# Kernel optimization log

Measured on AMD Instinct MI355X. Metric: run time of the kernel, lower is better.

The kernel has to match this reference:

```python
import jax, jax.numpy as jnp
import numpy as np

D_MODEL = 2048
D_INNER = 4096  # d_model * expand_factor
LN_EPS = 1e-5


def setup_inputs() -> dict:
    key = jax.random.key(0)
    k1, k2, k3, k4 = jax.random.split(key, 4)
    B, S = 2, 4096
    x = jax.random.normal(k1, (B, S, D_MODEL), dtype=jnp.float32)
    gamma = jnp.ones((D_MODEL,), dtype=jnp.float32)
    beta = jnp.zeros((D_MODEL,), dtype=jnp.float32)
    # nn.Linear-like small init to keep activations in-range
    W_in = jax.random.normal(k2, (2 * D_INNER, D_MODEL), dtype=jnp.float32) * 0.02
    W_out = jax.random.normal(k3, (D_MODEL, D_INNER), dtype=jnp.float32) * 0.02
    dt_min, dt_max = 0.001, 0.1
    dt = jax.random.uniform(k4, (D_INNER,), dtype=jnp.float32) * (dt_max - dt_min) + dt_min
    return {"x": x, "gamma": gamma, "beta": beta, "W_in": W_in, "W_out": W_out, "dt": dt}


def reference(x, gamma, beta, W_in, W_out, dt):
    # x: [B, S, D_MODEL]
    identity = x
    # LayerNorm over last dim
    mu = jnp.mean(x, axis=-1, keepdims=True)
    var = jnp.mean(jnp.square(x - mu), axis=-1, keepdims=True)
    xn = (x - mu) * jax.lax.rsqrt(var + LN_EPS) * gamma + beta
    # in_proj: [B, S, 2*D_INNER]
    projected = jnp.einsum("bsd,ed->bse", xn, W_in)
    z, gate = jnp.split(projected, 2, axis=-1)
    # z gated by sigmoid of clamped z (clamp only inside sigmoid)
    z_gated = z * jax.nn.sigmoid(jnp.clip(z, -15.0, 15.0))
    # temporal weighting by softmax(-dt) over d_inner
    dt_weights = jax.nn.softmax(-dt)  # [D_INNER]
    z_temporal = z_gated * dt_weights  # broadcast over [B, S, D_INNER]
    # gate path: silu on clamped gate
    output = z_temporal * jax.nn.silu(jnp.clip(gate, -15.0, 15.0))
    # out_proj back to d_model
    output = jnp.einsum("bse,de->bsd", output, W_out)
    return output + identity
```

## Files before the change

kernel.cpp:

```cpp
#include <hip/hip_runtime.h>
#include <cstdint>
#include <cstddef>

#define T_TOK 8192
#define DM    2048
#define DI    4096
#define TWO_DI 8192

typedef __attribute__((ext_vector_type(8))) short bf16x8;
typedef __attribute__((ext_vector_type(4))) float f32x4;

__device__ __forceinline__ unsigned short f2bf(float f) {
  union { float f; unsigned u; } c; c.f = f;
  unsigned u = c.u;
  unsigned r = (u + 0x7fffu + ((u >> 16) & 1u)) >> 16;
  return (unsigned short)r;
}

__global__ __launch_bounds__(256) void ln_kernel(
    const float* __restrict__ x, const float* __restrict__ gamma,
    const float* __restrict__ beta, unsigned short* __restrict__ xn) {
  const int t = blockIdx.x;
  const int tid = threadIdx.x;
  const float* row = x + (size_t)t * DM;
  float4 v0 = reinterpret_cast<const float4*>(row)[tid];
  float4 v1 = reinterpret_cast<const float4*>(row)[tid + 256];
  float s  = v0.x + v0.y + v0.z + v0.w + v1.x + v1.y + v1.z + v1.w;
  float ss = v0.x*v0.x + v0.y*v0.y + v0.z*v0.z + v0.w*v0.w
           + v1.x*v1.x + v1.y*v1.y + v1.z*v1.z + v1.w*v1.w;
  #pragma unroll
  for (int off = 32; off > 0; off >>= 1) {
    s  += __shfl_down(s, off);
    ss += __shfl_down(ss, off);
  }
  __shared__ float red[8];
  __shared__ float mu_s, inv_s;
  if ((tid & 63) == 0) { red[tid >> 6] = s; red[4 + (tid >> 6)] = ss; }
  __syncthreads();
  if (tid == 0) {
    float S  = red[0] + red[1] + red[2] + red[3];
    float SS = red[4] + red[5] + red[6] + red[7];
    float mu  = S * (1.0f / DM);
    float var = SS * (1.0f / DM) - mu * mu;
    mu_s = mu;
    inv_s = rsqrtf(var + 1e-5f);
  }
  __syncthreads();
  const float mu = mu_s, inv = inv_s;
  float4 g0 = reinterpret_cast<const float4*>(gamma)[tid];
  float4 b0 = reinterpret_cast<const float4*>(beta)[tid];
  float4 g1 = reinterpret_cast<const float4*>(gamma)[tid + 256];
  float4 b1 = reinterpret_cast<const float4*>(beta)[tid + 256];
  ushort4 o0, o1;
  o0.x = f2bf((v0.x - mu) * inv * g0.x + b0.x);
  o0.y = f2bf((v0.y - mu) * inv * g0.y + b0.y);
  o0.z = f2bf((v0.z - mu) * inv * g0.z + b0.z);
  o0.w = f2bf((v0.w - mu) * inv * g0.w + b0.w);
  o1.x = f2bf((v1.x - mu) * inv * g1.x + b1.x);
  o1.y = f2bf((v1.y - mu) * inv * g1.y + b1.y);
  o1.z = f2bf((v1.z - mu) * inv * g1.z + b1.z);
  o1.w = f2bf((v1.w - mu) * inv * g1.w + b1.w);
  reinterpret_cast<ushort4*>(xn + (size_t)t * DM)[tid]       = o0;
  reinterpret_cast<ushort4*>(xn + (size_t)t * DM)[tid + 256] = o1;
}

__global__ __launch_bounds__(256) void cvt_both(
    const float* __restrict__ a, unsigned short* __restrict__ oa, int n4a,
    const float* __restrict__ b, unsigned short* __restrict__ ob, int n4b) {
  int i = blockIdx.x * 256 + threadIdx.x;
  const float* src;
  unsigned short* dst;
  int idx;
  if (i < n4a) { src = a; dst = oa; idx = i; }
  else { idx = i - n4a; if (idx >= n4b) return; src = b; dst = ob; }
  float4 v = reinterpret_cast<const float4*>(src)[idx];
  ushort4 o;
  o.x = f2bf(v.x); o.y = f2bf(v.y); o.z = f2bf(v.z); o.w = f2bf(v.w);
  reinterpret_cast<ushort4*>(dst)[idx] = o;
}

__global__ __launch_bounds__(256) void dt_softmax(
    const float* __restrict__ dt, float* __restrict__ w) {
  const int tid = threadIdx.x;
  float e[16];
  float local = 0.f;
  #pragma unroll
  for (int i = 0; i < 16; ++i) {
    float v = __expf(-dt[i * 256 + tid]);
    e[i] = v;
    local += v;
  }
  #pragma unroll
  for (int off = 32; off > 0; off >>= 1) local += __shfl_down(local, off);
  __shared__ float red[4];
  __shared__ float tot;
  if ((tid & 63) == 0) red[tid >> 6] = local;
  __syncthreads();
  if (tid == 0) tot = red[0] + red[1] + red[2] + red[3];
  __syncthreads();
  const float inv = 1.f / tot;
  #pragma unroll
  for (int i = 0; i < 16; ++i) w[i * 256 + tid] = e[i] * inv;
}

__device__ __forceinline__ float actf(float z, float g, float w) {
  float zc = fminf(fmaxf(z, -15.f), 15.f);
  float sz = 1.f / (1.f + __expf(-zc));
  float gc = fminf(fmaxf(g, -15.f), 15.f);
  float sg = 1.f / (1.f + __expf(-gc));
  return z * sz * w * gc * sg;
}

#define BAR()    __builtin_amdgcn_s_barrier()
#define SCHED0() __builtin_amdgcn_sched_barrier(0)
#define PRIO1()  __builtin_amdgcn_s_setprio(1)
#define PRIO0()  __builtin_amdgcn_s_setprio(0)
#define WAIT_LGKM0() asm volatile("s_waitcnt lgkmcnt(0)" ::: "memory")
#define WAIT_VM6()   asm volatile("s_waitcnt vmcnt(6)" ::: "memory")

#define GLD16(gaddr, laddr) __builtin_amdgcn_global_load_lds(                 \
    (const __attribute__((address_space(1))) void*)(gaddr),                   \
    (__attribute__((address_space(3))) void*)(laddr), 16, 0, 0)

#define STAGE(ldsbase, gb, k0) do {                                           \
    GLD16((gb) + sOff  + (k0), &(ldsbase)[tid * 8]);                          \
    GLD16((gb) + sOff2 + (k0), &(ldsbase)[tid * 8 + 4096]);                   \
  } while (0)

#define TAIL() do { BAR(); WAIT_LGKM0(); SCHED0(); } while (0)

#define G1_NKT 32
#define G1_NIT 16

__global__ __launch_bounds__(512, 2) void gemm1_fused8(
    const unsigned short* __restrict__ A, const unsigned short* __restrict__ W,
    const float* __restrict__ dtw, unsigned short* __restrict__ act) {
  __shared__ unsigned short lA [2][256 * 64];
  __shared__ unsigned short lB1[2][128 * 64];
  __shared__ unsigned short lB2[2][128 * 64];

  const int tid  = threadIdx.x;
  const int lane = tid & 63;
  const int wmI  = (tid >> 6) >> 2;
  const int wnI  = (tid >> 6) & 3;
  const int tM = blockIdx.y * 256;
  const int tN = blockIdx.x * 128;

  const int r0   = lane & 15;
  const int hi4  = lane >> 4;
  const int swz0 = (hi4 ^ (r0 & 7)) << 3;
  const int swz1 = swz0 ^ 32;
  const int aRow0 = (wmI * 64 + r0) * 64;
  const int bRow  = (wnI * 32 + r0) * 64;

  const int srow = tid >> 3;
  const int scol = ((tid & 7) ^ (srow & 7)) << 3;
  const size_t sOff  = (size_t)srow * DM + scol;
  const size_t sOff2 = sOff + (size_t)64 * DM;

  const unsigned short* Ab    = A + (size_t)tM * DM;
  const unsigned short* Ab128 = Ab + (size_t)128 * DM;
  const unsigned short* B1b   = W + (size_t)tN * DM;
  const unsigned short* B2b   = W + (size_t)(tN + DI) * DM;

  f32x4 accZ[8][2], accG[8][2];
  #pragma unroll
  for (int i = 0; i < 8; ++i)
    #pragma unroll
    for (int j = 0; j < 2; ++j) {
      accZ[i][j] = f32x4{0.f, 0.f, 0.f, 0.f};
      accG[i][j] = f32x4{0.f, 0.f, 0.f, 0.f};
    }
  bf16x8 a0[4][2], a1[4][2], bz[2][2], bg[2][2];

#define G1_LDA0(b) do {                                                       \
    _Pragma("unroll") for (int i = 0; i < 4; ++i) {                           \
      a0[i][0] = *reinterpret_cast<const bf16x8*>(&lA[b][aRow0 + i*1024 + swz0]); \
      a0[i][1] = *reinterpret_cast<const bf16x8*>(&lA[b][aRow0 + i*1024 + swz1]); \
    } } while (0)
#define G1_LDA1(b) do {                                                       \
    _Pragma("unroll") for (int i = 0; i < 4; ++i) {                           \
      a1[i][0] = *reinterpret_cast<const bf16x8*>(&lA[b][8192 + aRow0 + i*1024 + swz0]); \
      a1[i][1] = *reinterpret_cast<const bf16x8*>(&lA[b][8192 + aRow0 + i*1024 + swz1]); \
    } } while (0)
#define G1_LDBZ(b) do {                                                       \
    _Pragma("unroll") for (int j = 0; j < 2; ++j) {                           \
      bz[j][0] = *reinterpret_cast<const bf16x8*>(&lB1[b][bRow + j*1024 + swz0]); \
      bz[j][1] = *reinterpret_cast<const bf16x8*>(&lB1[b][bRow + j*1024 + swz1]); \
    } } while (0)
#define G1_LDBG(b) do {                                                       \
    _Pragma("unroll") for (int j = 0; j < 2; ++j) {                           \
      bg[j][0] = *reinterpret_cast<const bf16x8*>(&lB2[b][bRow + j*1024 + swz0]); \
      bg[j][1] = *reinterpret_cast<const bf16x8*>(&lB2[b][bRow + j*1024 + swz1]); \
    } } while (0)
#define G1_Q(accA, ioff, af) do {                                             \
    PRIO1();                                                                  \
    _Pragma("unroll") for (int kh = 0; kh < 2; ++kh)                          \
      _Pragma("unroll") for (int i = 0; i < 4; ++i)                           \
        _Pragma("unroll") for (int j = 0; j < 2; ++j)                         \
          accA[(ioff)+i][j] = __builtin_amdgcn_mfma_f32_16x16x32_bf16(        \
              af[i][kh], G1_BF[j][kh], accA[(ioff)+i][j], 0, 0, 0);           \
    PRIO0(); SCHED0(); BAR();                                                 \
  } while (0)

  STAGE(lA[0],        Ab,    0);
  STAGE(lB1[0],       B1b,   0);
  STAGE(lB2[0],       B2b,   0);
  STAGE(&lA[0][8192], Ab128, 0);
  STAGE(lA[1],        Ab,    64);
  STAGE(lB1[1],       B1b,   64);
  STAGE(lB2[1],       B2b,   64);
  WAIT_VM6();
  BAR();

  #pragma unroll 1
  for (int t = 0; t < G1_NIT; ++t) {
    const int k1  = (2 * t + 1) * 64;
    const int kt2 = 2 * t + 2;
    const int kt3 = 2 * t + 3;
    const int k2 = (kt2 < G1_NKT ? kt2 : G1_NKT - 1) * 64;
    const int k3 = (kt3 < G1_NKT ? kt3 : G1_NKT - 1) * 64;

#define G1_BF bz
    G1_LDA0(0); G1_LDBZ(0);
    STAGE(&lA[1][8192], Ab128, k1);
    TAIL(); G1_Q(accZ, 0, a0);
#undef G1_BF
#define G1_BF bg
    G1_LDBG(0);
    STAGE(lA[0], Ab, k2);
    TAIL(); G1_Q(accG, 0, a0);
    G1_LDA1(0);
    STAGE(lB1[0], B1b, k2);
    TAIL(); G1_Q(accG, 4, a1);
#undef G1_BF
#define G1_BF bz
    STAGE(lB2[0], B2b, k2);
    WAIT_VM6();
    TAIL(); G1_Q(accZ, 4, a1);
#undef G1_BF

#define G1_BF bz
    G1_LDA0(1); G1_LDBZ(1);
    STAGE(&lA[0][8192], Ab128, k2);
    TAIL(); G1_Q(accZ, 0, a0);
#undef G1_BF
#define G1_BF bg
    G1_LDBG(1);
    STAGE(lA[1], Ab, k3);
    TAIL(); G1_Q(accG, 0, a0);
    G1_LDA1(1);
    STAGE(lB1[1], B1b, k3);
    TAIL(); G1_Q(accG, 4, a1);
#undef G1_BF
#define G1_BF bz
    STAGE(lB2[1], B2b, k3);
    WAIT_VM6();
    TAIL(); G1_Q(accZ, 4, a1);
#undef G1_BF
  }

  const int qr   = hi4 << 2;
  const int colb = tN + wnI * 32 + r0;
  const float w0 = dtw[colb];
  const float w1 = dtw[colb + 16];
  #pragma unroll
  for (int i = 0; i < 8; ++i) {
    const int rowb = tM + wmI * 64 + ((i & 3) << 4) + ((i >> 2) << 7) + qr;
    #pragma unroll
    for (int r = 0; r < 4; ++r) {
      const size_t base = (size_t)(rowb + r) * DI + colb;
      act[base]      = f2bf(actf(accZ[i][0][r], accG[i][0][r], w0));
      act[base + 16] = f2bf(actf(accZ[i][1][r], accG[i][1][r], w1));
    }
  }
#undef G1_LDA0
#undef G1_LDA1
#undef G1_LDBZ
#undef G1_LDBG
#undef G1_Q
}

#define G2_NKT 64
#define G2_NIT 32

__global__ __launch_bounds__(512, 2) void gemm2_res8(
    const unsigned short* __restrict__ A, const unsigned short* __restrict__ Bm,
    float* __restrict__ out, const float* __restrict__ ident) {
  __shared__ unsigned short lA[2][256 * 64];
  __shared__ unsigned short lB[2][256 * 64];

  const int tid  = threadIdx.x;
  const int lane = tid & 63;
  const int wmI  = (tid >> 6) >> 2;
  const int wnI  = (tid >> 6) & 3;
  const int tM = blockIdx.y * 256;
  const int tN = blockIdx.x * 256;

  const int r0   = lane & 15;
  const int hi4  = lane >> 4;
  const int swz0 = (hi4 ^ (r0 & 7)) << 3;
  const int swz1 = swz0 ^ 32;
  const int aRow0 = (wmI * 64 + r0) * 64;
  const int bRow  = (wnI * 32 + r0) * 64;

  const int srow = tid >> 3;
  const int scol = ((tid & 7) ^ (srow & 7)) << 3;
  const size_t sOff  = (size_t)srow * DI + scol;
  const size_t sOff2 = sOff + (size_t)64 * DI;

  const unsigned short* Ab    = A + (size_t)tM * DI;
  const unsigned short* Ab128 = Ab + (size_t)128 * DI;
  const unsigned short* Bb    = Bm + (size_t)tN * DI;
  const unsigned short* Bb128 = Bb + (size_t)128 * DI;

  f32x4 acc[8][4];
  #pragma unroll
  for (int i = 0; i < 8; ++i)
    #pragma unroll
    for (int j = 0; j < 4; ++j) acc[i][j] = f32x4{0.f, 0.f, 0.f, 0.f};
  bf16x8 a0[4][2], a1[4][2], b0[2][2], b1[2][2];

#define G2_LDA0(b) do {                                                       \
    _Pragma("unroll") for (int i = 0; i < 4; ++i) {                           \
      a0[i][0] = *reinterpret_cast<const bf16x8*>(&lA[b][aRow0 + i*1024 + swz0]); \
      a0[i][1] = *reinterpret_cast<const bf16x8*>(&lA[b][aRow0 + i*1024 + swz1]); \
    } } while (0)
#define G2_LDA1(b) do {                                                       \
    _Pragma("unroll") for (int i = 0; i < 4; ++i) {                           \
      a1[i][0] = *reinterpret_cast<const bf16x8*>(&lA[b][8192 + aRow0 + i*1024 + swz0]); \
      a1[i][1] = *reinterpret_cast<const bf16x8*>(&lA[b][8192 + aRow0 + i*1024 + swz1]); \
    } } while (0)
#define G2_LDB0(b) do {                                                       \
    _Pragma("unroll") for (int j = 0; j < 2; ++j) {                           \
      b0[j][0] = *reinterpret_cast<const bf16x8*>(&lB[b][bRow + j*1024 + swz0]); \
      b0[j][1] = *reinterpret_cast<const bf16x8*>(&lB[b][bRow + j*1024 + swz1]); \
    } } while (0)
#define G2_LDB1(b) do {                                                       \
    _Pragma("unroll") for (int j = 0; j < 2; ++j) {                           \
      b1[j][0] = *reinterpret_cast<const bf16x8*>(&lB[b][8192 + bRow + j*1024 + swz0]); \
      b1[j][1] = *reinterpret_cast<const bf16x8*>(&lB[b][8192 + bRow + j*1024 + swz1]); \
    } } while (0)
#define G2_Q(ioff, joff, af, bf) do {                                         \
    PRIO1();                                                                  \
    _Pragma("unroll") for (int kh = 0; kh < 2; ++kh)                          \
      _Pragma("unroll") for (int i = 0; i < 4; ++i)                           \
        _Pragma("unroll") for (int j = 0; j < 2; ++j)                         \
          acc[(ioff)+i][(joff)+j] = __builtin_amdgcn_mfma_f32_16x16x32_bf16(  \
              af[i][kh], bf[j][kh], acc[(ioff)+i][(joff)+j], 0, 0, 0);        \
    PRIO0(); SCHED0(); BAR();                                                 \
  } while (0)

  STAGE(lA[0],        Ab,    0);
  STAGE(lB[0],        Bb,    0);
  STAGE(&lB[0][8192], Bb128, 0);
  STAGE(&lA[0][8192], Ab128, 0);
  STAGE(lA[1],        Ab,    64);
  STAGE(lB[1],        Bb,    64);
  STAGE(&lB[1][8192], Bb128, 64);
  WAIT_VM6();
  BAR();

  #pragma unroll 1
  for (int t = 0; t < G2_NIT; ++t) {
    const int k1  = (2 * t + 1) * 64;
    const int kt2 = 2 * t + 2;
    const int kt3 = 2 * t + 3;
    const int k2 = (kt2 < G2_NKT ? kt2 : G2_NKT - 1) * 64;
    const int k3 = (kt3 < G2_NKT ? kt3 : G2_NKT - 1) * 64;

    G2_LDA0(0); G2_LDB0(0);
    STAGE(&lA[1][8192], Ab128, k1);
    TAIL(); G2_Q(0, 0, a0, b0);
    G2_LDB1(0);
    STAGE(lA[0], Ab, k2);
    TAIL(); G2_Q(0, 2, a0, b1);
    G2_LDA1(0);
    STAGE(lB[0], Bb, k2);
    TAIL(); G2_Q(4, 2, a1, b1);
    STAGE(&lB[0][8192], Bb128, k2);
    WAIT_VM6();
    TAIL(); G2_Q(4, 0, a1, b0);

    G2_LDA0(1); G2_LDB0(1);
    STAGE(&lA[0][8192], Ab128, k2);
    TAIL(); G2_Q(0, 0, a0, b0);
    G2_LDB1(1);
    STAGE(lA[1], Ab, k3);
    TAIL(); G2_Q(0, 2, a0, b1);
    G2_LDA1(1);
    STAGE(lB[1], Bb, k3);
    TAIL(); G2_Q(4, 2, a1, b1);
    STAGE(&lB[1][8192], Bb128, k3);
    WAIT_VM6();
    TAIL(); G2_Q(4, 0, a1, b0);
  }

  const int qr   = hi4 << 2;
  const int colb = tN + wnI * 32 + r0;
  #pragma unroll
  for (int i = 0; i < 8; ++i) {
    const int rowb = tM + wmI * 64 + ((i & 3) << 4) + ((i >> 2) << 7) + qr;
    #pragma unroll
    for (int r = 0; r < 4; ++r) {
      const size_t rowoff = (size_t)(rowb + r) * DM;
      #pragma unroll
      for (int j = 0; j < 4; ++j) {
        const size_t idx = rowoff + colb + ((j & 1) << 4) + ((j >> 1) << 7);
        out[idx] = acc[i][j][r] + ident[idx];
      }
    }
  }
#undef G2_LDA0
#undef G2_LDA1
#undef G2_LDB0
#undef G2_LDB1
#undef G2_Q
}

extern "C" void kernel_launch(void* const* d_in, const int* in_sizes, int n_in,
                              void* d_out, int out_size, void* d_ws, size_t ws_size,
                              hipStream_t stream) {
  const float* x     = (const float*)d_in[0];
  const float* gamma = (const float*)d_in[1];
  const float* beta  = (const float*)d_in[2];
  const float* W_in  = (const float*)d_in[3];
  const float* W_out = (const float*)d_in[4];
  const float* dt    = (const float*)d_in[5];
  float* out = (float*)d_out;

  char* ws = (char*)d_ws;
  unsigned short* xn     = (unsigned short*)(ws);
  unsigned short* win_b  = (unsigned short*)(ws + ((size_t)32 << 20));
  unsigned short* wout_b = (unsigned short*)(ws + ((size_t)64 << 20));
  float*          dtw    = (float*)(ws + ((size_t)80 << 20));
  unsigned short* act    = (unsigned short*)(ws + ((size_t)96 << 20));

  const int n4_in  = TWO_DI * DM / 4;
  const int n4_out = DM * DI / 4;

  ln_kernel<<<T_TOK, 256, 0, stream>>>(x, gamma, beta, xn);
  cvt_both<<<(n4_in + n4_out + 255) / 256, 256, 0, stream>>>(
      W_in, win_b, n4_in, W_out, wout_b, n4_out);
  dt_softmax<<<1, 256, 0, stream>>>(dt, dtw);

  gemm1_fused8<<<dim3(DI / 128, T_TOK / 256), 512, 0, stream>>>(
      xn, win_b, dtw, act);

  gemm2_res8<<<dim3(DM / 256, T_TOK / 256), 512, 0, stream>>>(
      act, wout_b, out, x);
}
```

Before: 586.9 us.

## Split LDS fragment loads by k-half with partial lgkmcnt waits in both GEMMs

Both GEMM kernels now issue LDS fragment reads per k-half. Each quarter waits only on the lgkmcnt needed for the first half of its MFMAs, so those MFMAs can start while the second-half reads are still in flight. The barrier that sat before the LDS wait is also dropped, leaving one barrier per quarter after compute instead of two. This is meant to hide LDS read latency and cut barrier stalls. The risk is that the hand-tuned wait counts must match the compiler's issued instruction order, or the reordering may not help.

After: 602.5 us. +2.6%, slower.

```diff
diff --git a/kernel.cpp b/kernel.cpp
--- a/kernel.cpp
+++ b/kernel.cpp
@@ -115,7 +115,7 @@
 #define SCHED0() __builtin_amdgcn_sched_barrier(0)
 #define PRIO1()  __builtin_amdgcn_s_setprio(1)
 #define PRIO0()  __builtin_amdgcn_s_setprio(0)
-#define WAIT_LGKM0() asm volatile("s_waitcnt lgkmcnt(0)" ::: "memory")
+#define WAIT_LGKM(n) asm volatile("s_waitcnt lgkmcnt(" #n ")" ::: "memory")
 #define WAIT_VM6()   asm volatile("s_waitcnt vmcnt(6)" ::: "memory")
 
 #define GLD16(gaddr, laddr) __builtin_amdgcn_global_load_lds(                 \
@@ -126,8 +126,6 @@
     GLD16((gb) + sOff  + (k0), &(ldsbase)[tid * 8]);                          \
     GLD16((gb) + sOff2 + (k0), &(ldsbase)[tid * 8 + 4096]);                   \
   } while (0)
-
-#define TAIL() do { BAR(); WAIT_LGKM0(); SCHED0(); } while (0)
 
 #define G1_NKT 32
 #define G1_NIT 16
@@ -173,34 +171,33 @@
     }
   bf16x8 a0[4][2], a1[4][2], bz[2][2], bg[2][2];
 
-#define G1_LDA0(b) do {                                                       \
-    _Pragma("unroll") for (int i = 0; i < 4; ++i) {                           \
-      a0[i][0] = *reinterpret_cast<const bf16x8*>(&lA[b][aRow0 + i*1024 + swz0]); \
-      a0[i][1] = *reinterpret_cast<const bf16x8*>(&lA[b][aRow0 + i*1024 + swz1]); \
-    } } while (0)
-#define G1_LDA1(b) do {                                                       \
-    _Pragma("unroll") for (int i = 0; i < 4; ++i) {                           \
-      a1[i][0] = *reinterpret_cast<const bf16x8*>(&lA[b][8192 + aRow0 + i*1024 + swz0]); \
-      a1[i][1] = *reinterpret_cast<const bf16x8*>(&lA[b][8192 + aRow0 + i*1024 + swz1]); \
-    } } while (0)
-#define G1_LDBZ(b) do {                                                       \
-    _Pragma("unroll") for (int j = 0; j < 2; ++j) {                           \
-      bz[j][0] = *reinterpret_cast<const bf16x8*>(&lB1[b][bRow + j*1024 + swz0]); \
-      bz[j][1] = *reinterpret_cast<const bf16x8*>(&lB1[b][bRow + j*1024 + swz1]); \
-    } } while (0)
-#define G1_LDBG(b) do {                                                       \
-    _Pragma("unroll") for (int j = 0; j < 2; ++j) {                           \
-      bg[j][0] = *reinterpret_cast<const bf16x8*>(&lB2[b][bRow + j*1024 + swz0]); \
-      bg[j][1] = *reinterpret_cast<const bf16x8*>(&lB2[b][bRow + j*1024 + swz1]); \
-    } } while (0)
-#define G1_Q(accA, ioff, af) do {                                             \
+#define G1_LDA0K(b, kh) do {                                                  \
+    _Pragma("unroll") for (int i = 0; i < 4; ++i)                             \
+      a0[i][kh] = *reinterpret_cast<const bf16x8*>(                           \
+          &lA[b][aRow0 + i*1024 + ((kh) ? swz1 : swz0)]);                     \
+  } while (0)
+#define G1_LDA1K(b, kh) do {                                                  \
+    _Pragma("unroll") for (int i = 0; i < 4; ++i)                             \
+      a1[i][kh] = *reinterpret_cast<const bf16x8*>(                           \
+          &lA[b][8192 + aRow0 + i*1024 + ((kh) ? swz1 : swz0)]);              \
+  } while (0)
+#define G1_LDBZK(b, kh) do {                                                  \
+    _Pragma("unroll") for (int j = 0; j < 2; ++j)                             \
+      bz[j][kh] = *reinterpret_cast<const bf16x8*>(                           \
+          &lB1[b][bRow + j*1024 + ((kh) ? swz1 : swz0)]);                     \
+  } while (0)
+#define G1_LDBGK(b, kh) do {                                                  \
+    _Pragma("unroll") for (int j = 0; j < 2; ++j)                             \
+      bg[j][kh] = *reinterpret_cast<const bf16x8*>(                           \
+          &lB2[b][bRow + j*1024 + ((kh) ? swz1 : swz0)]);                     \
+  } while (0)
+#define G1_H(accA, ioff, af, bf, kh) do {                                     \
     PRIO1();                                                                  \
-    _Pragma("unroll") for (int kh = 0; kh < 2; ++kh)                          \
-      _Pragma("unroll") for (int i = 0; i < 4; ++i)                           \
-        _Pragma("unroll") for (int j = 0; j < 2; ++j)                         \
-          accA[(ioff)+i][j] = __builtin_amdgcn_mfma_f32_16x16x32_bf16(        \
-              af[i][kh], G1_BF[j][kh], accA[(ioff)+i][j], 0, 0, 0);           \
-    PRIO0(); SCHED0(); BAR();                                                 \
+    _Pragma("unroll") for (int i = 0; i < 4; ++i)                             \
+      _Pragma("unroll") for (int j = 0; j < 2; ++j)                           \
+        accA[(ioff)+i][j] = __builtin_amdgcn_mfma_f32_16x16x32_bf16(          \
+            af[i][kh], bf[j][kh], accA[(ioff)+i][j], 0, 0, 0);                \
+    PRIO0(); SCHED0();                                                        \
   } while (0)
 
   STAGE(lA[0],        Ab,    0);
@@ -221,43 +218,59 @@
     const int k2 = (kt2 < G1_NKT ? kt2 : G1_NKT - 1) * 64;
     const int k3 = (kt3 < G1_NKT ? kt3 : G1_NKT - 1) * 64;
 
-#define G1_BF bz
-    G1_LDA0(0); G1_LDBZ(0);
+    G1_LDA0K(0,0); G1_LDBZK(0,0); G1_LDA0K(0,1); G1_LDBZK(0,1);
     STAGE(&lA[1][8192], Ab128, k1);
-    TAIL(); G1_Q(accZ, 0, a0);
-#undef G1_BF
-#define G1_BF bg
-    G1_LDBG(0);
+    WAIT_LGKM(6); SCHED0();
+    G1_H(accZ, 0, a0, bz, 0);
+    WAIT_LGKM(0); SCHED0();
+    G1_H(accZ, 0, a0, bz, 1);
+    BAR();
+    G1_LDBGK(0,0); G1_LDBGK(0,1);
     STAGE(lA[0], Ab, k2);
-    TAIL(); G1_Q(accG, 0, a0);
-    G1_LDA1(0);
+    WAIT_LGKM(2); SCHED0();
+    G1_H(accG, 0, a0, bg, 0);
+    WAIT_LGKM(0); SCHED0();
+    G1_H(accG, 0, a0, bg, 1);
+    BAR();
+    G1_LDA1K(0,0); G1_LDA1K(0,1);
     STAGE(lB1[0], B1b, k2);
-    TAIL(); G1_Q(accG, 4, a1);
-#undef G1_BF
-#define G1_BF bz
+    WAIT_LGKM(4); SCHED0();
+    G1_H(accG, 4, a1, bg, 0);
+    WAIT_LGKM(0); SCHED0();
+    G1_H(accG, 4, a1, bg, 1);
+    BAR();
     STAGE(lB2[0], B2b, k2);
-    WAIT_VM6();
-    TAIL(); G1_Q(accZ, 4, a1);
-#undef G1_BF
-
-#define G1_BF bz
-    G1_LDA0(1); G1_LDBZ(1);
+    WAIT_VM6(); SCHED0();
+    G1_H(accZ, 4, a1, bz, 0);
+    G1_H(accZ, 4, a1, bz, 1);
+    BAR();
+
+    G1_LDA0K(1,0); G1_LDBZK(1,0); G1_LDA0K(1,1); G1_LDBZK(1,1);
     STAGE(&lA[0][8192], Ab128, k2);
-    TAIL(); G1_Q(accZ, 0, a0);
-#undef G1_BF
-#define G1_BF bg
-    G1_LDBG(1);
+    WAIT_LGKM(6); SCHED0();
+    G1_H(accZ, 0, a0, bz, 0);
+    WAIT_LGKM(0); SCHED0();
+    G1_H(accZ, 0, a0, bz, 1);
+    BAR();
+    G1_LDBGK(1,0); G1_LDBGK(1,1);
     STAGE(lA[1], Ab, k3);
-    TAIL(); G1_Q(accG, 0, a0);
-    G1_LDA1(1);
+    WAIT_LGKM(2); SCHED0();
+    G1_H(accG, 0, a0, bg, 0);
+    WAIT_LGKM(0); SCHED0();
+    G1_H(accG, 0, a0, bg, 1);
+    BAR();
+    G1_LDA1K(1,0); G1_LDA1K(1,1);
     STAGE(lB1[1], B1b, k3);
-    TAIL(); G1_Q(accG, 4, a1);
-#undef G1_BF
-#define G1_BF bz
+    WAIT_LGKM(4); SCHED0();
+    G1_H(accG, 4, a1, bg, 0);
+    WAIT_LGKM(0); SCHED0();
+    G1_H(accG, 4, a1, bg, 1);
+    BAR();
     STAGE(lB2[1], B2b, k3);
-    WAIT_VM6();
-    TAIL(); G1_Q(accZ, 4, a1);
-#undef G1_BF
+    WAIT_VM6(); SCHED0();
+    G1_H(accZ, 4, a1, bz, 0);
+    G1_H(accZ, 4, a1, bz, 1);
+    BAR();
   }
 
   const int qr   = hi4 << 2;
@@ -274,11 +287,11 @@
       act[base + 16] = f2bf(actf(accZ[i][1][r], accG[i][1][r], w1));
     }
   }
-#undef G1_LDA0
-#undef G1_LDA1
-#undef G1_LDBZ
-#undef G1_LDBG
-#undef G1_Q
+#undef G1_LDA0K
+#undef G1_LDA1K
+#undef G1_LDBZK
+#undef G1_LDBGK
+#undef G1_H
 }
 
 #define G2_NKT 64
@@ -321,34 +334,33 @@
     for (int j = 0; j < 4; ++j) acc[i][j] = f32x4{0.f, 0.f, 0.f, 0.f};
   bf16x8 a0[4][2], a1[4][2], b0[2][2], b1[2][2];
 
-#define G2_LDA0(b) do {                                                       \
-    _Pragma("unroll") for (int i = 0; i < 4; ++i) {                           \
-      a0[i][0] = *reinterpret_cast<const bf16x8*>(&lA[b][aRow0 + i*1024 + swz0]); \
-      a0[i][1] = *reinterpret_cast<const bf16x8*>(&lA[b][aRow0 + i*1024 + swz1]); \
-    } } while (0)
-#define G2_LDA1(b) do {                                                       \
-    _Pragma("unroll") for (int i = 0; i < 4; ++i) {                           \
-      a1[i][0] = *reinterpret_cast<const bf16x8*>(&lA[b][8192 + aRow0 + i*1024 + swz0]); \
-      a1[i][1] = *reinterpret_cast<const bf16x8*>(&lA[b][8192 + aRow0 + i*1024 + swz1]); \
-    } } while (0)
-#define G2_LDB0(b) do {                                                       \
-    _Pragma("unroll") for (int j = 0; j < 2; ++j) {                           \
-      b0[j][0] = *reinterpret_cast<const bf16x8*>(&lB[b][bRow + j*1024 + swz0]); \
-      b0[j][1] = *reinterpret_cast<const bf16x8*>(&lB[b][bRow + j*1024 + swz1]); \
-    } } while (0)
-#define G2_LDB1(b) do {                                                       \
-    _Pragma("unroll") for (int j = 0; j < 2; ++j) {                           \
-      b1[j][0] = *reinterpret_cast<const bf16x8*>(&lB[b][8192 + bRow + j*1024 + swz0]); \
-      b1[j][1] = *reinterpret_cast<const bf16x8*>(&lB[b][8192 + bRow + j*1024 + swz1]); \
-    } } while (0)
-#define G2_Q(ioff, joff, af, bf) do {                                         \
+#define G2_LDA0K(b, kh) do {                                                  \
+    _Pragma("unroll") for (int i = 0; i < 4; ++i)                             \
+      a0[i][kh] = *reinterpret_cast<const bf16x8*>(                           \
+          &lA[b][aRow0 + i*1024 + ((kh) ? swz1 : swz0)]);                     \
+  } while (0)
+#define G2_LDA1K(b, kh) do {                                                  \
+    _Pragma("unroll") for (int i = 0; i < 4; ++i)                             \
+      a1[i][kh] = *reinterpret_cast<const bf16x8*>(                           \
+          &lA[b][8192 + aRow0 + i*1024 + ((kh) ? swz1 : swz0)]);              \
+  } while (0)
+#define G2_LDB0K(b, kh) do {                                                  \
+    _Pragma("unroll") for (int j = 0; j < 2; ++j)                             \
+      b0[j][kh] = *reinterpret_cast<const bf16x8*>(                           \
+          &lB[b][bRow + j*1024 + ((kh) ? swz1 : swz0)]);                      \
+  } while (0)
+#define G2_LDB1K(b, kh) do {                                                  \
+    _Pragma("unroll") for (int j = 0; j < 2; ++j)                             \
+      b1[j][kh] = *reinterpret_cast<const bf16x8*>(                           \
+          &lB[b][8192 + bRow + j*1024 + ((kh) ? swz1 : swz0)]);               \
+  } while (0)
+#define G2_H(ioff, joff, af, bf, kh) do {                                     \
     PRIO1();                                                                  \
-    _Pragma("unroll") for (int kh = 0; kh < 2; ++kh)                          \
-      _Pragma("unroll") for (int i = 0; i < 4; ++i)                           \
-        _Pragma("unroll") for (int j = 0; j < 2; ++j)                         \
-          acc[(ioff)+i][(joff)+j] = __builtin_amdgcn_mfma_f32_16x16x32_bf16(  \
-              af[i][kh], bf[j][kh], acc[(ioff)+i][(joff)+j], 0, 0, 0);        \
-    PRIO0(); SCHED0(); BAR();                                                 \
+    _Pragma("unroll") for (int i = 0; i < 4; ++i)                             \
+      _Pragma("unroll") for (int j = 0; j < 2; ++j)                           \
+        acc[(ioff)+i][(joff)+j] = __builtin_amdgcn_mfma_f32_16x16x32_bf16(    \
+            af[i][kh], bf[j][kh], acc[(ioff)+i][(joff)+j], 0, 0, 0);          \
+    PRIO0(); SCHED0();                                                        \
   } while (0)
 
   STAGE(lA[0],        Ab,    0);
@@ -369,31 +381,59 @@
     const int k2 = (kt2 < G2_NKT ? kt2 : G2_NKT - 1) * 64;
     const int k3 = (kt3 < G2_NKT ? kt3 : G2_NKT - 1) * 64;
 
-    G2_LDA0(0); G2_LDB0(0);
+    G2_LDA0K(0,0); G2_LDB0K(0,0); G2_LDA0K(0,1); G2_LDB0K(0,1);
     STAGE(&lA[1][8192], Ab128, k1);
-    TAIL(); G2_Q(0, 0, a0, b0);
-    G2_LDB1(0);
+    WAIT_LGKM(6); SCHED0();
+    G2_H(0, 0, a0, b0, 0);
+    WAIT_LGKM(0); SCHED0();
+    G2_H(0, 0, a0, b0, 1);
+    BAR();
+    G2_LDB1K(0,0); G2_LDB1K(0,1);
     STAGE(lA[0], Ab, k2);
-    TAIL(); G2_Q(0, 2, a0, b1);
-    G2_LDA1(0);
+    WAIT_LGKM(2); SCHED0();
+    G2_H(0, 2, a0, b1, 0);
+    WAIT_LGKM(0); SCHED0();
+    G2_H(0, 2, a0, b1, 1);
+    BAR();
+    G2_LDA1K(0,0); G2_LDA1K(0,1);
     STAGE(lB[0], Bb, k2);
-    TAIL(); G2_Q(4, 2, a1, b1);
+    WAIT_LGKM(4); SCHED0();
+    G2_H(4, 2, a1, b1, 0);
+    WAIT_LGKM(0); SCHED0();
+    G2_H(4, 2, a1, b1, 1);
+    BAR();
     STAGE(&lB[0][8192], Bb128, k2);
-    WAIT_VM6();
-    TAIL(); G2_Q(4, 0, a1, b0);
-
-    G2_LDA0(1); G2_LDB0(1);
+    WAIT_VM6(); SCHED0();
+    G2_H(4, 0, a1, b0, 0);
+    G2_H(4, 0, a1, b0, 1);
+    BAR();
+
+    G2_LDA0K(1,0); G2_LDB0K(1,0); G2_LDA0K(1,1); G2_LDB0K(1,1);
     STAGE(&lA[0][8192], Ab128, k2);
-    TAIL(); G2_Q(0, 0, a0, b0);
-    G2_LDB1(1);
+    WAIT_LGKM(6); SCHED0();
+    G2_H(0, 0, a0, b0, 0);
+    WAIT_LGKM(0); SCHED0();
+    G2_H(0, 0, a0, b0, 1);
+    BAR();
+    G2_LDB1K(1,0); G2_LDB1K(1,1);
     STAGE(lA[1], Ab, k3);
-    TAIL(); G2_Q(0, 2, a0, b1);
-    G2_LDA1(1);
+    WAIT_LGKM(2); SCHED0();
+    G2_H(0, 2, a0, b1, 0);
+    WAIT_LGKM(0); SCHED0();
+    G2_H(0, 2, a0, b1, 1);
+    BAR();
+    G2_LDA1K(1,0); G2_LDA1K(1,1);
     STAGE(lB[1], Bb, k3);
-    TAIL(); G2_Q(4, 2, a1, b1);
+    WAIT_LGKM(4); SCHED0();
+    G2_H(4, 2, a1, b1, 0);
+    WAIT_LGKM(0); SCHED0();
+    G2_H(4, 2, a1, b1, 1);
+    BAR();
     STAGE(&lB[1][8192], Bb128, k3);
-    WAIT_VM6();
-    TAIL(); G2_Q(4, 0, a1, b0);
+    WAIT_VM6(); SCHED0();
+    G2_H(4, 0, a1, b0, 0);
+    G2_H(4, 0, a1, b0, 1);
+    BAR();
   }
 
   const int qr   = hi4 << 2;
@@ -411,11 +451,11 @@
       }
     }
   }
-#undef G2_LDA0
-#undef G2_LDA1
-#undef G2_LDB0
-#undef G2_LDB1
-#undef G2_Q
+#undef G2_LDA0K
+#undef G2_LDA1K
+#undef G2_LDB0K
+#undef G2_LDB1K
+#undef G2_H
 }
 
 extern "C" void kernel_launch(void* const* d_in, const int* in_sizes, int n_in,
```
